# Kernel optimization log

Measured on AMD Instinct MI355X. Metric: run time of the kernel, lower is better.

The kernel has to match this reference:

```python
import jax, jax.numpy as jnp
import numpy as np
from jax import lax

# ---- static config (from init_kwargs / input_specs) ----
B, NB, C, F = 16, 8192, 3, 64   # batches, points-per-batch, coord dim, feat dim
RATIO, K = 0.125, 16
M = int(RATIO * NB)


def setup_inputs() -> dict:
    key = jax.random.key(0)
    kx, kp = jax.random.split(key)
    x = jax.random.normal(kx, (B * NB, F), dtype=jnp.float32)
    pos = jax.random.normal(kp, (B * NB, C), dtype=jnp.float32)
    batch = (jnp.arange(B * NB, dtype=jnp.int32) // NB).astype(jnp.int32)
    return {"x": x, "pos": pos, "batch": batch}


def _fps_single(pos_b):
    """Sequential farthest point sampling on (NB, C), deterministic start at 0.
    Returns (M,) int32 indices into pos_b."""
    n = pos_b.shape[0]

    def step(carry, _):
        min_d2, last = carry
        d2 = jnp.sum((pos_b - pos_b[last]) ** 2, axis=-1)   # (NB,)
        min_d2 = jnp.minimum(min_d2, d2)
        nxt = jnp.argmax(min_d2).astype(jnp.int32)
        return (min_d2, nxt), last

    init = (jnp.full((n,), jnp.finfo(pos_b.dtype).max, dtype=pos_b.dtype),
            jnp.int32(0))
    _, idx = lax.scan(step, init, None, length=M)
    return idx  # (M,)


def reference(x, pos, batch):
    # batch ids are block-constant (batch[i] = i // NB), so per-batch views are
    # simple reshapes -- same semantics as torch_cluster's batched fps/knn.
    pos_b = pos.reshape(B, NB, C)

    # --- farthest point sampling per batch ---
    fps_idx = jax.vmap(_fps_single)(pos_b)                            # (B, M)
    centroids = jnp.take_along_axis(pos_b, fps_idx[..., None], axis=1)  # (B, M, C)

    # --- k-NN: squared distances centroids -> all points of same batch ---
    d2 = (jnp.sum(centroids ** 2, axis=-1)[..., None]
          - 2.0 * jnp.einsum('bmc,bnc->bmn', centroids, pos_b)
          + jnp.sum(pos_b ** 2, axis=-1)[:, None, :])                 # (B, M, NB)
    _, nn_idx = lax.top_k(-d2, K)                                     # (B, M, K)

    # gather neighbor coordinates (== pos[groups_idx[1]])
    groups = jax.vmap(lambda p, i: p[i])(pos_b, nn_idx.reshape(B, M * K))  # (B, M*K, C)

    return centroids.reshape(B * M, C), groups.reshape(B * M * K, C)
```

## Files before the change

kernel.cpp:

```cpp
#include <hip/hip_runtime.h>
#include <float.h>
#include <math.h>

#define B_   16
#define NB_  8192
#define M_   1024
#define K_   16


typedef float v2f __attribute__((ext_vector_type(2)));

#define FPS_T 256
#define PPT   32
#define NPAIR (PPT/2)
#define NWAVE (FPS_T/64)

#define KNN_T   256
#define CHUNK   1024
#define GRP     8
#define BCAP    16
#define BSTRIDE 17

#define FPS_BLOCKS B_
#define C012_WGS   (B_*3)
#define SPLIT3     8

__device__ __forceinline__ void topk_insert(float d2, int pi, float val[16], int idx[16])
{
    int r = 0;
    #pragma unroll
    for (int j = 0; j < 16; ++j) r += (val[j] <= d2) ? 1 : 0;
    #pragma unroll
    for (int j = 15; j >= 1; --j) {
        bool sh = (j > r);
        val[j] = sh ? val[j-1] : val[j];
        idx[j] = sh ? idx[j-1] : idx[j];
    }
    #pragma unroll
    for (int j = 0; j < 16; ++j) {
        bool pl = (j == r);
        val[j] = pl ? d2 : val[j];
        idx[j] = pl ? pi : idx[j];
    }
}

__global__ __launch_bounds__(256, 1) void fused_kernel(
    const float* __restrict__ pos, float* __restrict__ cent,
    float* __restrict__ groups, unsigned long long* __restrict__ partials,
    unsigned int* __restrict__ progress, int split3)
{
    #pragma clang fp contract(off)
    __shared__ float4 spts[NB_];
    __shared__ unsigned long long wkey[2][NWAVE];

    const int blk = blockIdx.x;
    const int t   = threadIdx.x;

    if (blk < FPS_BLOCKS) {
        const int b = blk;
        const float* pb = pos + (size_t)b * NB_ * 3;
        float* cb = cent + (size_t)b * M_ * 3;

        for (int p = t; p < NB_; p += FPS_T) {
            const float* s = pb + (size_t)p * 3;
            spts[p] = make_float4(s[0], s[1], s[2], 0.0f);
        }

        v2f px2[NPAIR], py2[NPAIR], pz2[NPAIR], md2[NPAIR];
        #pragma unroll
        for (int jj = 0; jj < NPAIR; ++jj) {
            const float* s0 = pb + (size_t)(t*PPT + 2*jj) * 3;
            px2[jj] = (v2f){s0[0], s0[3]};
            py2[jj] = (v2f){s0[1], s0[4]};
            pz2[jj] = (v2f){s0[2], s0[5]};
            md2[jj] = (v2f){FLT_MAX, FLT_MAX};
        }
        __syncthreads();

        float lx = pb[0], ly = pb[1], lz = pb[2];
        float c0x=0,c0y=0,c0z=0,c1x=0,c1y=0,c1z=0,c2x=0,c2y=0,c2z=0,c3x=0,c3y=0,c3z=0;

        for (int m = 0; m < M_; ++m) {
            if (t == (m >> 2)) {
                const int sl = m & 3;
                if      (sl == 0) { c0x=lx; c0y=ly; c0z=lz; }
                else if (sl == 1) { c1x=lx; c1y=ly; c1z=lz; }
                else if (sl == 2) { c2x=lx; c2y=ly; c2z=lz; }
                else              { c3x=lx; c3y=ly; c3z=lz; }
            }

            if ((m & 255) == 255) {
                const int cg = m >> 8;
                if ((t >> 6) == cg) {
                    float4* o = (float4*)(cb + (size_t)t * 12);
                    o[0] = make_float4(c0x, c0y, c0z, c1x);
                    o[1] = make_float4(c1y, c1z, c2x, c2y);
                    o[2] = make_float4(c2z, c3x, c3y, c3z);
                    if ((t & 63) == 0)
                        __hip_atomic_store(&progress[b], (unsigned)(cg + 1),
                                           __ATOMIC_RELEASE, __HIP_MEMORY_SCOPE_AGENT);
                }
            }
            if (m == M_ - 1) break;

            const v2f lxv = {lx,lx}, lyv = {ly,ly}, lzv = {lz,lz};
            v2f bmax2 = {-1.0f, -1.0f};
            #pragma unroll
            for (int jj = 0; jj < NPAIR; ++jj) {
                v2f dx = px2[jj] - lxv;
                v2f dy = py2[jj] - lyv;
                v2f dz = pz2[jj] - lzv;
                v2f d2 = (dx*dx + dy*dy) + dz*dz;
                v2f mj = __builtin_elementwise_min(md2[jj], d2);
                md2[jj] = mj;
                bmax2 = __builtin_elementwise_max(bmax2, mj);
            }
            float bm = fmaxf(bmax2.x, bmax2.y);

            float v = bm;
            {
                int vi;
                vi = __builtin_amdgcn_update_dpp(__float_as_int(v), __float_as_int(v), 0xB1,  0xF, 0xF, false);
                v = fmaxf(v, __int_as_float(vi));
                vi = __builtin_amdgcn_update_dpp(__float_as_int(v), __float_as_int(v), 0x4E,  0xF, 0xF, false);
                v = fmaxf(v, __int_as_float(vi));
                vi = __builtin_amdgcn_update_dpp(__float_as_int(v), __float_as_int(v), 0x141, 0xF, 0xF, false);
                v = fmaxf(v, __int_as_float(vi));
                vi = __builtin_amdgcn_update_dpp(__float_as_int(v), __float_as_int(v), 0x140, 0xF, 0xF, false);
                v = fmaxf(v, __int_as_float(vi));
                vi = __builtin_amdgcn_update_dpp(__float_as_int(v), __float_as_int(v), 0x142, 0xF, 0xF, false);
                v = fmaxf(v, __int_as_float(vi));
                vi = __builtin_amdgcn_update_dpp(__float_as_int(v), __float_as_int(v), 0x143, 0xF, 0xF, false);
                v = fmaxf(v, __int_as_float(vi));
            }
            const float wv = __int_as_float(__builtin_amdgcn_readlane(__float_as_int(v), 63));

            int jp = -1;
            #pragma unroll
            for (int jj = NPAIR - 1; jj >= 0; --jj) {
                if (md2[jj].y == wv) jp = 2*jj + 1;
                if (md2[jj].x == wv) jp = 2*jj;
            }
            const unsigned long long mk = __ballot(jp >= 0);
            const int wl = (int)__ffsll(mk) - 1;
            const int gi = __builtin_amdgcn_readlane(t*PPT + jp, wl);

            const int par = m & 1;
            if ((t & 63) == 0)
                wkey[par][t >> 6] = ((unsigned long long)__float_as_uint(wv) << 32) |
                                    (unsigned int)(~gi);
            __syncthreads();

            unsigned long long kk = wkey[par][0];
            #pragma unroll
            for (int w = 1; w < NWAVE; ++w) {
                const unsigned long long e = wkey[par][w];
                kk = (e > kk) ? e : kk;
            }
            const int best = (int)(~(unsigned int)kk);

            const float4 c = spts[best];
            lx = c.x; ly = c.y; lz = c.z;
        }
        return;
    }

    const int r = blk - FPS_BLOCKS;
    int b, cg, sp, span, pbase, direct;
    if (r < C012_WGS) {
        b = r / 3; cg = r % 3; sp = 0; span = NB_; pbase = 0; direct = 1;
    } else {
        const int r3 = r - C012_WGS;
        cg = 3;
        if (split3 == 1) { b = r3;      sp = 0;       span = NB_;        pbase = 0;        direct = 1; }
        else             { b = r3 >> 3; sp = r3 & 7;  span = NB_/SPLIT3; pbase = sp*span;  direct = 0; }
    }

    if (t == 0) {
        while (__hip_atomic_load(&progress[b], __ATOMIC_ACQUIRE,
                                 __HIP_MEMORY_SCOPE_AGENT) < (unsigned)(cg + 1))
            __builtin_amdgcn_s_sleep(64);
    }
    __syncthreads();

    float4* kpts = spts;
    unsigned long long* sbuf = (unsigned long long*)(spts + CHUNK);

    const float* pb = pos + (size_t)b * NB_ * 3;
    const int nchunks = span / CHUNK;
    const int mg = b * M_ + cg * KNN_T + t;
    const float cx = cent[(size_t)mg*3+0];
    const float cy = cent[(size_t)mg*3+1];
    const float cz = cent[(size_t)mg*3+2];
    const float cn2 = (cx*cx + cy*cy) + cz*cz;

    float val[16]; int idx[16];
    #pragma unroll
    for (int j = 0; j < 16; ++j) { val[j] = FLT_MAX; idx[j] = 0; }
    float tau = FLT_MAX;
    int cnt = 0;
    unsigned long long* mybuf = sbuf + t * BSTRIDE;

    for (int c = 0; c < nchunks; ++c) {
        const int ps = pbase + c * CHUNK;
        __syncthreads();
        for (int p = t; p < CHUNK; p += KNN_T) {
            const float* s = pb + (size_t)(ps + p) * 3;
            float x = s[0], y = s[1], z = s[2];
            float pn2 = (x*x + y*y) + z*z;
            kpts[p] = make_float4(x, y, z, pn2);
        }
        __syncthreads();

        for (int p0 = 0; p0 < CHUNK; p0 += GRP) {
            if (__any(cnt > BCAP - GRP)) {
                int n = cnt; cnt = 0;
                for (int i = 0; i < n; ++i) {
                    unsigned long long e = mybuf[i];
                    float d = __uint_as_float((unsigned int)(e >> 32));
                    int pi  = (int)(e & 0xFFFFFFFFu);
                    if (d < val[15]) topk_insert(d, pi, val, idx);
                }
                tau = val[15];
            }
            float4 q[GRP];
            #pragma unroll
            for (int i = 0; i < GRP; ++i) q[i] = kpts[p0 + i];
            float d2v[GRP];
            #pragma unroll
            for (int i = 0; i < GRP; ++i) {
                float dot = __builtin_fmaf(cz, q[i].z,
                            __builtin_fmaf(cy, q[i].y, cx * q[i].x));
                d2v[i] = (cn2 - 2.0f*dot) + q[i].w;
            }
            #pragma unroll
            for (int i = 0; i < GRP; ++i) {
                if (d2v[i] < tau) {
                    mybuf[cnt] = ((unsigned long long)__float_as_uint(d2v[i]) << 32) |
                                 (unsigned int)(ps + p0 + i);
                    ++cnt;
                }
            }
        }
    }
    {
        int n = cnt;
        for (int i = 0; i < n; ++i) {
            unsigned long long e = mybuf[i];
            float d = __uint_as_float((unsigned int)(e >> 32));
            int pi  = (int)(e & 0xFFFFFFFFu);
            if (d < val[15]) topk_insert(d, pi, val, idx);
        }
    }

    if (!direct) {
        unsigned long long* o = partials + ((size_t)(b * 256 + t) * SPLIT3 + sp) * 16;
        #pragma unroll
        for (int kq = 0; kq < 16; ++kq)
            o[kq] = ((unsigned long long)__float_as_uint(val[kq]) << 32) | (unsigned int)idx[kq];
    } else {
        float* g = groups + (size_t)mg * K_ * 3;
        #pragma unroll
        for (int kq = 0; kq < 16; ++kq) {
            const float* s = pb + (size_t)idx[kq] * 3;
            g[kq*3+0] = s[0]; g[kq*3+1] = s[1]; g[kq*3+2] = s[2];
        }
    }
}

__global__ __launch_bounds__(256, 2) void knn_merge3(const float* __restrict__ pos,
    const unsigned long long* __restrict__ partials, float* __restrict__ groups)
{
    const int g  = blockIdx.x * 256 + threadIdx.x;
    const int b  = g >> 8;
    const int tt = g & 255;
    const float* pb = pos + (size_t)b * NB_ * 3;

    float val[16]; int idx[16];
    #pragma unroll
    for (int j = 0; j < 16; ++j) { val[j] = FLT_MAX; idx[j] = 0; }
    for (int sp = 0; sp < SPLIT3; ++sp) {
        const unsigned long long* l = partials + ((size_t)(b * 256 + tt) * SPLIT3 + sp) * 16;
        #pragma unroll
        for (int kq = 0; kq < 16; ++kq) {
            unsigned long long e = l[kq];
            float d = __uint_as_float((unsigned int)(e >> 32));
            int pi  = (int)(e & 0xFFFFFFFFu);
            if (d < val[15]) topk_insert(d, pi, val, idx);
        }
    }
    const int mg = b * M_ + 3 * KNN_T + tt;
    float* o = groups + (size_t)mg * K_ * 3;
    #pragma unroll
    for (int kq = 0; kq < 16; ++kq) {
        const float* s = pb + (size_t)idx[kq] * 3;
        o[kq*3+0] = s[0]; o[kq*3+1] = s[1]; o[kq*3+2] = s[2];
    }
}

__global__ __launch_bounds__(FPS_T, 1) void fps_kernel(const float* __restrict__ pos,
                                                       float* __restrict__ cent)
{
    #pragma clang fp contract(off)
    const int b = blockIdx.x;
    const int t = threadIdx.x;
    const float* pb = pos + (size_t)b * NB_ * 3;
    float* cb = cent + (size_t)b * M_ * 3;

    __shared__ float4 spts[NB_];
    __shared__ unsigned long long wkey[2][NWAVE];

    for (int p = t; p < NB_; p += FPS_T) {
        const float* s = pb + (size_t)p * 3;
        spts[p] = make_float4(s[0], s[1], s[2], 0.0f);
    }

    v2f px2[NPAIR], py2[NPAIR], pz2[NPAIR], md2[NPAIR];
    #pragma unroll
    for (int jj = 0; jj < NPAIR; ++jj) {
        const float* s0 = pb + (size_t)(t*PPT + 2*jj) * 3;
        px2[jj] = (v2f){s0[0], s0[3]};
        py2[jj] = (v2f){s0[1], s0[4]};
        pz2[jj] = (v2f){s0[2], s0[5]};
        md2[jj] = (v2f){FLT_MAX, FLT_MAX};
    }
    __syncthreads();

    float lx = pb[0], ly = pb[1], lz = pb[2];
    float c0x=0,c0y=0,c0z=0,c1x=0,c1y=0,c1z=0,c2x=0,c2y=0,c2z=0,c3x=0,c3y=0,c3z=0;

    for (int m = 0; m < M_; ++m) {
        if (t == (m >> 2)) {
            const int sl = m & 3;
            if      (sl == 0) { c0x=lx; c0y=ly; c0z=lz; }
            else if (sl == 1) { c1x=lx; c1y=ly; c1z=lz; }
            else if (sl == 2) { c2x=lx; c2y=ly; c2z=lz; }
            else              { c3x=lx; c3y=ly; c3z=lz; }
        }
        if (m == M_ - 1) break;

        const v2f lxv = {lx,lx}, lyv = {ly,ly}, lzv = {lz,lz};
        v2f bmax2 = {-1.0f, -1.0f};
        #pragma unroll
        for (int jj = 0; jj < NPAIR; ++jj) {
            v2f dx = px2[jj] - lxv;
            v2f dy = py2[jj] - lyv;
            v2f dz = pz2[jj] - lzv;
            v2f d2 = (dx*dx + dy*dy) + dz*dz;
            v2f mj = __builtin_elementwise_min(md2[jj], d2);
            md2[jj] = mj;
            bmax2 = __builtin_elementwise_max(bmax2, mj);
        }
        float bm = fmaxf(bmax2.x, bmax2.y);

        float v = bm;
        {
            int vi;
            vi = __builtin_amdgcn_update_dpp(__float_as_int(v), __float_as_int(v), 0xB1,  0xF, 0xF, false);
            v = fmaxf(v, __int_as_float(vi));
            vi = __builtin_amdgcn_update_dpp(__float_as_int(v), __float_as_int(v), 0x4E,  0xF, 0xF, false);
            v = fmaxf(v, __int_as_float(vi));
            vi = __builtin_amdgcn_update_dpp(__float_as_int(v), __float_as_int(v), 0x141, 0xF, 0xF, false);
            v = fmaxf(v, __int_as_float(vi));
            vi = __builtin_amdgcn_update_dpp(__float_as_int(v), __float_as_int(v), 0x140, 0xF, 0xF, false);
            v = fmaxf(v, __int_as_float(vi));
            vi = __builtin_amdgcn_update_dpp(__float_as_int(v), __float_as_int(v), 0x142, 0xF, 0xF, false);
            v = fmaxf(v, __int_as_float(vi));
            vi = __builtin_amdgcn_update_dpp(__float_as_int(v), __float_as_int(v), 0x143, 0xF, 0xF, false);
            v = fmaxf(v, __int_as_float(vi));
        }
        const float wv = __int_as_float(__builtin_amdgcn_readlane(__float_as_int(v), 63));

        int jp = -1;
        #pragma unroll
        for (int jj = NPAIR - 1; jj >= 0; --jj) {
            if (md2[jj].y == wv) jp = 2*jj + 1;
            if (md2[jj].x == wv) jp = 2*jj;
        }
        const unsigned long long mk = __ballot(jp >= 0);
        const int wl = (int)__ffsll(mk) - 1;
        const int gi = __builtin_amdgcn_readlane(t*PPT + jp, wl);

        const int par = m & 1;
        if ((t & 63) == 0)
            wkey[par][t >> 6] = ((unsigned long long)__float_as_uint(wv) << 32) |
                                (unsigned int)(~gi);
        __syncthreads();

        unsigned long long kk = wkey[par][0];
        #pragma unroll
        for (int w = 1; w < NWAVE; ++w) {
            const unsigned long long e = wkey[par][w];
            kk = (e > kk) ? e : kk;
        }
        const int best = (int)(~(unsigned int)kk);

        const float4 c = spts[best];
        lx = c.x; ly = c.y; lz = c.z;
    }

    {
        float4* o = (float4*)(cb + (size_t)t * 12);
        o[0] = make_float4(c0x, c0y, c0z, c1x);
        o[1] = make_float4(c1y, c1z, c2x, c2y);
        o[2] = make_float4(c2z, c3x, c3y, c3z);
    }
}

__global__ __launch_bounds__(KNN_T, 2) void knn_kernel(const float* __restrict__ pos,
    const float* __restrict__ cent, float* __restrict__ groups,
    unsigned long long* __restrict__ partials, int nsplit)
{
    #pragma clang fp contract(off)
    __shared__ float4 kpts[CHUNK];
    __shared__ unsigned long long sbuf[KNN_T * BSTRIDE];

    const int wg = blockIdx.x;
    const int t  = threadIdx.x;
    const int per_b = 4 * nsplit;
    const int b  = wg / per_b;
    const int r  = wg % per_b;
    const int cg = r / nsplit;
    const int sp = r % nsplit;
    const int span  = NB_ / nsplit;
    const int pbase = sp * span;
    const int nchunks = span / CHUNK;

    const float* pb = pos + (size_t)b * NB_ * 3;
    const int mg = b * M_ + cg * KNN_T + t;
    const float cx = cent[(size_t)mg*3+0];
    const float cy = cent[(size_t)mg*3+1];
    const float cz = cent[(size_t)mg*3+2];
    const float cn2 = (cx*cx + cy*cy) + cz*cz;

    float val[16]; int idx[16];
    #pragma unroll
    for (int j = 0; j < 16; ++j) { val[j] = FLT_MAX; idx[j] = 0; }
    float tau = FLT_MAX;
    int cnt = 0;
    unsigned long long* mybuf = sbuf + t * BSTRIDE;

    for (int c = 0; c < nchunks; ++c) {
        const int ps = pbase + c * CHUNK;
        __syncthreads();
        for (int p = t; p < CHUNK; p += KNN_T) {
            const float* s = pb + (size_t)(ps + p) * 3;
            float x = s[0], y = s[1], z = s[2];
            float pn2 = (x*x + y*y) + z*z;
            kpts[p] = make_float4(x, y, z, pn2);
        }
        __syncthreads();

        for (int p0 = 0; p0 < CHUNK; p0 += GRP) {
            if (__any(cnt > BCAP - GRP)) {
                int n = cnt; cnt = 0;
                for (int i = 0; i < n; ++i) {
                    unsigned long long e = mybuf[i];
                    float d = __uint_as_float((unsigned int)(e >> 32));
                    int pi  = (int)(e & 0xFFFFFFFFu);
                    if (d < val[15]) topk_insert(d, pi, val, idx);
                }
                tau = val[15];
            }
            float4 q[GRP];
            #pragma unroll
            for (int i = 0; i < GRP; ++i) q[i] = kpts[p0 + i];
            float d2v[GRP];
            #pragma unroll
            for (int i = 0; i < GRP; ++i) {
                float dot = __builtin_fmaf(cz, q[i].z,
                            __builtin_fmaf(cy, q[i].y, cx * q[i].x));
                d2v[i] = (cn2 - 2.0f*dot) + q[i].w;
            }
            #pragma unroll
            for (int i = 0; i < GRP; ++i) {
                if (d2v[i] < tau) {
                    mybuf[cnt] = ((unsigned long long)__float_as_uint(d2v[i]) << 32) |
                                 (unsigned int)(ps + p0 + i);
                    ++cnt;
                }
            }
        }
    }
    {
        int n = cnt;
        for (int i = 0; i < n; ++i) {
            unsigned long long e = mybuf[i];
            float d = __uint_as_float((unsigned int)(e >> 32));
            int pi  = (int)(e & 0xFFFFFFFFu);
            if (d < val[15]) topk_insert(d, pi, val, idx);
        }
    }

    if (nsplit > 1) {
        unsigned long long* o = partials + ((size_t)mg * nsplit + sp) * 16;
        #pragma unroll
        for (int kq = 0; kq < 16; ++kq)
            o[kq] = ((unsigned long long)__float_as_uint(val[kq]) << 32) | (unsigned int)idx[kq];
    } else {
        float* g = groups + (size_t)mg * K_ * 3;
        #pragma unroll
        for (int kq = 0; kq < 16; ++kq) {
            const float* s = pb + (size_t)idx[kq] * 3;
            g[kq*3+0] = s[0]; g[kq*3+1] = s[1]; g[kq*3+2] = s[2];
        }
    }
}

__global__ __launch_bounds__(256, 2) void knn_merge(const float* __restrict__ pos,
    const unsigned long long* __restrict__ partials, float* __restrict__ groups,
    int nsplit)
{
    const int mg = blockIdx.x * 256 + threadIdx.x;
    const int b  = mg >> 10;
    const float* pb = pos + (size_t)b * NB_ * 3;

    float val[16]; int idx[16];
    #pragma unroll
    for (int j = 0; j < 16; ++j) { val[j] = FLT_MAX; idx[j] = 0; }
    for (int sp = 0; sp < nsplit; ++sp) {
        const unsigned long long* l = partials + ((size_t)mg * nsplit + sp) * 16;
        #pragma unroll
        for (int kq = 0; kq < 16; ++kq) {
            unsigned long long e = l[kq];
            float d = __uint_as_float((unsigned int)(e >> 32));
            int pi  = (int)(e & 0xFFFFFFFFu);
            if (d < val[15]) topk_insert(d, pi, val, idx);
        }
    }
    float* g = groups + (size_t)mg * K_ * 3;
    #pragma unroll
    for (int kq = 0; kq < 16; ++kq) {
        const float* s = pb + (size_t)idx[kq] * 3;
        g[kq*3+0] = s[0]; g[kq*3+1] = s[1]; g[kq*3+2] = s[2];
    }
}

extern "C" void kernel_launch(void* const* d_in, const int* in_sizes, int n_in,
                              void* d_out, int out_size, void* d_ws, size_t ws_size,
                              hipStream_t stream)
{
    (void)in_sizes; (void)n_in; (void)out_size;
    const float* pos = (const float*)d_in[1];
    float* out    = (float*)d_out;
    float* cent   = out;
    float* groups = out + (size_t)B_ * M_ * 3;

    const size_t FLAGS = 256;
    const size_t PART  = (size_t)B_ * 256 * SPLIT3 * 16 *
                         sizeof(unsigned long long);

    if (ws_size >= FLAGS) {
        const int split3 = (ws_size >= FLAGS + PART) ? SPLIT3 : 1;
        unsigned int* progress = (unsigned int*)d_ws;
        unsigned long long* partials = (unsigned long long*)((char*)d_ws + FLAGS);

        hipMemsetAsync(d_ws, 0, FLAGS, stream);

        const int grid = FPS_BLOCKS + C012_WGS +
                         (split3 == SPLIT3 ? B_ * SPLIT3 : B_);
        fused_kernel<<<grid, 256, 0, stream>>>(pos, cent, groups, partials,
                                               progress, split3);
        if (split3 == SPLIT3)
            knn_merge3<<<(B_ * 256) / 256, 256, 0, stream>>>(pos, partials, groups);
    } else {
        fps_kernel<<<B_, FPS_T, 0, stream>>>(pos, cent);
        const size_t lst = (size_t)B_ * M_ * 16 * sizeof(unsigned long long);
        int nsplit = (ws_size >= 8*lst) ? 8 : (ws_size >= 4*lst) ? 4 :
                     (ws_size >= 2*lst) ? 2 : 1;
        knn_kernel<<<B_ * 4 * nsplit, KNN_T, 0, stream>>>(pos, cent, groups,
                                                          (unsigned long long*)d_ws, nsplit);
        if (nsplit > 1)
            knn_merge<<<(B_ * M_) / 256, 256, 0, stream>>>(pos,
                (const unsigned long long*)d_ws, groups, nsplit);
    }
}
```

Baseline: 1.446 ms.

## Split later kNN centroid groups geometrically and prefetch first chunk before waiting on FPS

The kNN work for each batch is now split unevenly. Centroid group 0 scans all points directly, while groups 1, 2 and 3 are split into 2, 4 and 8 point ranges. This shrinks the work left after each FPS progress flag so the tail after FPS finishes gets shorter, and a generalized merge kernel combines the partial top-k lists. The first point chunk is also staged into shared memory before spinning on the progress flag, which hides load latency behind the wait. In exchange it uses more blocks, a larger partial workspace, and a merge pass over more centroids, and it drops the path that ran without the partials workspace.

```diff
diff --git a/kernel.cpp b/kernel.cpp
--- a/kernel.cpp
+++ b/kernel.cpp
@@ -22,8 +22,9 @@
 #define BSTRIDE 17
 
 #define FPS_BLOCKS B_
-#define C012_WGS   (B_*3)
-#define SPLIT3     8
+#define WGS_PER_B  15
+#define KNN_BLOCKS (B_ * WGS_PER_B)
+#define MAXSP      8
 
 __device__ __forceinline__ void topk_insert(float d2, int pi, float val[16], int idx[16])
 {
@@ -47,7 +48,7 @@
 __global__ __launch_bounds__(256, 1) void fused_kernel(
     const float* __restrict__ pos, float* __restrict__ cent,
     float* __restrict__ groups, unsigned long long* __restrict__ partials,
-    unsigned int* __restrict__ progress, int split3)
+    unsigned int* __restrict__ progress)
 {
     #pragma clang fp contract(off)
     __shared__ float4 spts[NB_];
@@ -166,14 +167,28 @@
     }
 
     const int r = blk - FPS_BLOCKS;
-    int b, cg, sp, span, pbase, direct;
-    if (r < C012_WGS) {
-        b = r / 3; cg = r % 3; sp = 0; span = NB_; pbase = 0; direct = 1;
-    } else {
-        const int r3 = r - C012_WGS;
-        cg = 3;
-        if (split3 == 1) { b = r3;      sp = 0;       span = NB_;        pbase = 0;        direct = 1; }
-        else             { b = r3 >> 3; sp = r3 & 7;  span = NB_/SPLIT3; pbase = sp*span;  direct = 0; }
+    const int b = r / WGS_PER_B;
+    const int w = r % WGS_PER_B;
+    int cg, sp;
+    if      (w == 0) { cg = 0; sp = 0; }
+    else if (w < 3)  { cg = 1; sp = w - 1; }
+    else if (w < 7)  { cg = 2; sp = w - 3; }
+    else             { cg = 3; sp = w - 7; }
+    const int span   = NB_ >> cg;
+    const int pbase  = sp * span;
+    const int direct = (cg == 0);
+    const int nchunks = span / CHUNK;
+
+    float4* kpts = spts;
+    unsigned long long* sbuf = (unsigned long long*)(spts + CHUNK);
+
+    const float* pb = pos + (size_t)b * NB_ * 3;
+
+    for (int p = t; p < CHUNK; p += KNN_T) {
+        const float* s = pb + (size_t)(pbase + p) * 3;
+        float x = s[0], y = s[1], z = s[2];
+        float pn2 = (x*x + y*y) + z*z;
+        kpts[p] = make_float4(x, y, z, pn2);
     }
 
     if (t == 0) {
@@ -183,11 +198,6 @@
     }
     __syncthreads();
 
-    float4* kpts = spts;
-    unsigned long long* sbuf = (unsigned long long*)(spts + CHUNK);
-
-    const float* pb = pos + (size_t)b * NB_ * 3;
-    const int nchunks = span / CHUNK;
     const int mg = b * M_ + cg * KNN_T + t;
     const float cx = cent[(size_t)mg*3+0];
     const float cy = cent[(size_t)mg*3+1];
@@ -203,14 +213,6 @@
 
     for (int c = 0; c < nchunks; ++c) {
         const int ps = pbase + c * CHUNK;
-        __syncthreads();
-        for (int p = t; p < CHUNK; p += KNN_T) {
-            const float* s = pb + (size_t)(ps + p) * 3;
-            float x = s[0], y = s[1], z = s[2];
-            float pn2 = (x*x + y*y) + z*z;
-            kpts[p] = make_float4(x, y, z, pn2);
-        }
-        __syncthreads();
 
         for (int p0 = 0; p0 < CHUNK; p0 += GRP) {
             if (__any(cnt > BCAP - GRP)) {
@@ -242,6 +244,18 @@
                 }
             }
         }
+
+        if (c + 1 < nchunks) {
+            __syncthreads();
+            const int ns = pbase + (c + 1) * CHUNK;
+            for (int p = t; p < CHUNK; p += KNN_T) {
+                const float* s = pb + (size_t)(ns + p) * 3;
+                float x = s[0], y = s[1], z = s[2];
+                float pn2 = (x*x + y*y) + z*z;
+                kpts[p] = make_float4(x, y, z, pn2);
+            }
+            __syncthreads();
+        }
     }
     {
         int n = cnt;
@@ -254,7 +268,8 @@
     }
 
     if (!direct) {
-        unsigned long long* o = partials + ((size_t)(b * 256 + t) * SPLIT3 + sp) * 16;
+        unsigned long long* o = partials +
+            ((((size_t)(b * 3 + (cg - 1)) * 256 + t) * MAXSP) + sp) * 16;
         #pragma unroll
         for (int kq = 0; kq < 16; ++kq)
             o[kq] = ((unsigned long long)__float_as_uint(val[kq]) << 32) | (unsigned int)idx[kq];
@@ -268,19 +283,25 @@
     }
 }
 
-__global__ __launch_bounds__(256, 2) void knn_merge3(const float* __restrict__ pos,
+__global__ __launch_bounds__(256, 2) void knn_merge_c(const float* __restrict__ pos,
     const unsigned long long* __restrict__ partials, float* __restrict__ groups)
 {
     const int g  = blockIdx.x * 256 + threadIdx.x;
-    const int b  = g >> 8;
-    const int tt = g & 255;
+    const int b  = g / 768;
+    const int u  = g % 768;
+    const int cg = 1 + u / 256;
+    const int tt = u % 256;
+    const int nsp = 1 << cg;
     const float* pb = pos + (size_t)b * NB_ * 3;
 
+    const unsigned long long* base = partials +
+        (((size_t)(b * 3 + (cg - 1)) * 256 + tt) * MAXSP) * 16;
+
     float val[16]; int idx[16];
     #pragma unroll
     for (int j = 0; j < 16; ++j) { val[j] = FLT_MAX; idx[j] = 0; }
-    for (int sp = 0; sp < SPLIT3; ++sp) {
-        const unsigned long long* l = partials + ((size_t)(b * 256 + tt) * SPLIT3 + sp) * 16;
+    for (int sp = 0; sp < nsp; ++sp) {
+        const unsigned long long* l = base + sp * 16;
         #pragma unroll
         for (int kq = 0; kq < 16; ++kq) {
             unsigned long long e = l[kq];
@@ -289,7 +310,7 @@
             if (d < val[15]) topk_insert(d, pi, val, idx);
         }
     }
-    const int mg = b * M_ + 3 * KNN_T + tt;
+    const int mg = b * M_ + cg * 256 + tt;
     float* o = groups + (size_t)mg * K_ * 3;
     #pragma unroll
     for (int kq = 0; kq < 16; ++kq) {
@@ -547,22 +568,17 @@
     float* groups = out + (size_t)B_ * M_ * 3;
 
     const size_t FLAGS = 256;
-    const size_t PART  = (size_t)B_ * 256 * SPLIT3 * 16 *
-                         sizeof(unsigned long long);
-
-    if (ws_size >= FLAGS) {
-        const int split3 = (ws_size >= FLAGS + PART) ? SPLIT3 : 1;
+    const size_t PART  = (size_t)B_ * 768 * MAXSP * 16 * sizeof(unsigned long long);
+
+    if (ws_size >= FLAGS + PART) {
         unsigned int* progress = (unsigned int*)d_ws;
         unsigned long long* partials = (unsigned long long*)((char*)d_ws + FLAGS);
 
         hipMemsetAsync(d_ws, 0, FLAGS, stream);
 
-        const int grid = FPS_BLOCKS + C012_WGS +
-                         (split3 == SPLIT3 ? B_ * SPLIT3 : B_);
-        fused_kernel<<<grid, 256, 0, stream>>>(pos, cent, groups, partials,
-                                               progress, split3);
-        if (split3 == SPLIT3)
-            knn_merge3<<<(B_ * 256) / 256, 256, 0, stream>>>(pos, partials, groups);
+        fused_kernel<<<FPS_BLOCKS + KNN_BLOCKS, 256, 0, stream>>>(pos, cent, groups,
+                                                                  partials, progress);
+        knn_merge_c<<<(B_ * 768) / 256, 256, 0, stream>>>(pos, partials, groups);
     } else {
         fps_kernel<<<B_, FPS_T, 0, stream>>>(pos, cent);
         const size_t lst = (size_t)B_ * M_ * 16 * sizeof(unsigned long long);
```

Result: faster. 1.267 ms (-12.4%).
